# Kernel optimization log

Measured on AMD Instinct MI355X. Metric: run time of the kernel, lower is better.

Reference implementation:

```python
import jax, jax.numpy as jnp
import numpy as np

MUL = 32          # channel multiplicity of node features (32x0e + 32x1o)
N_SPEC = 4        # one-hot species dim (node_attrs = 4x0e)
N_EMB = 8         # radial (bessel) embedding dim
HID = 8           # invariant_neurons
TP_W = 4 * MUL    # tp.weight_numel: 4 'uvu' paths, 32 weights each
INV_SQRT3 = 0.5773502691896258


def setup_inputs() -> dict:
    key = jax.random.key(0)
    ks = jax.random.split(key, 13)
    N, E = 50000, 800000
    node_features = jax.random.normal(ks[0], (N, 4 * MUL), jnp.float32)
    node_attrs = jax.random.uniform(ks[1], (N, N_SPEC), dtype=jnp.float32)
    edge_index = jax.random.randint(ks[2], (2, E), 0, N)
    edge_attrs = jax.random.normal(ks[3], (E, 4), jnp.float32)          # SH: [0e | 1o(3)]
    edge_embedding = jax.random.uniform(ks[4], (E, N_EMB), dtype=jnp.float32)
    # learned parameters
    W1_s = jax.random.normal(ks[5], (MUL, MUL), jnp.float32)            # linear_1 scalar block
    W1_v = jax.random.normal(ks[6], (MUL, MUL), jnp.float32)            # linear_1 vector block
    fc_w1 = jax.random.normal(ks[7], (N_EMB, HID), jnp.float32)         # radial MLP layer 1
    fc_w2 = jax.random.normal(ks[8], (HID, TP_W), jnp.float32)          # radial MLP -> tp weights
    W2_s = jax.random.normal(ks[9], (2 * MUL, MUL), jnp.float32)        # linear_2: 64x0e -> 32x0e
    W2_v = jax.random.normal(ks[10], (2 * MUL, MUL), jnp.float32)       # linear_2: 64x1o -> 32x1o
    Wsc_s = jax.random.normal(ks[11], (MUL, N_SPEC, MUL), jnp.float32)  # sc: 0e x 0e -> 0e (uvw)
    Wsc_v = jax.random.normal(ks[12], (MUL, N_SPEC, MUL), jnp.float32)  # sc: 1o x 0e -> 1o (uvw)
    return dict(node_features=node_features, node_attrs=node_attrs,
                edge_attrs=edge_attrs, edge_embedding=edge_embedding,
                W1_s=W1_s, W1_v=W1_v, fc_w1=fc_w1, fc_w2=fc_w2,
                W2_s=W2_s, W2_v=W2_v, Wsc_s=Wsc_s, Wsc_v=Wsc_v,
                edge_index=edge_index)


def reference(node_features, node_attrs, edge_attrs, edge_embedding,
              W1_s, W1_v, fc_w1, fc_w2, W2_s, W2_v, Wsc_s, Wsc_v, edge_index):
    N = node_features.shape[0]
    edge_src = edge_index[1]
    edge_dst = edge_index[0]

    # split node features into scalar (32x0e) and vector (32x1o) blocks
    s = node_features[:, :MUL]                       # [N, 32]
    v = node_features[:, MUL:].reshape(N, MUL, 3)    # [N, 32, 3]

    # --- self-connection: FullyConnectedTensorProduct(features, node_attrs) ---
    sc_norm = 1.0 / jnp.sqrt(jnp.float32(MUL * N_SPEC))
    sc_s = jnp.einsum('nu,na,uaw->nw', s, node_attrs, Wsc_s) * sc_norm
    sc_v = jnp.einsum('nui,na,uaw->nwi', v, node_attrs, Wsc_v) * sc_norm

    # --- linear_1 (per-irrep linear, fan-in normalized) ---
    l1 = 1.0 / jnp.sqrt(jnp.float32(MUL))
    s1 = (s @ W1_s) * l1                                   # [N, 32]
    v1 = jnp.einsum('nui,uw->nwi', v, W1_v) * l1           # [N, 32, 3]

    # --- radial MLP: edge_embedding -> per-edge tp weights (silu) ---
    h = jax.nn.silu((edge_embedding @ fc_w1) / jnp.sqrt(jnp.float32(N_EMB)))
    w = (h @ fc_w2) / jnp.sqrt(jnp.float32(HID))           # [E, 128]
    w0, w1, w2, w3 = w[:, :MUL], w[:, MUL:2*MUL], w[:, 2*MUL:3*MUL], w[:, 3*MUL:]

    # --- gather source-node features per edge ---
    ss = s1[edge_src]                                      # [E, 32]
    vv = v1[edge_src]                                      # [E, 32, 3]
    a0 = edge_attrs[:, 0]                                  # [E]    0e SH
    a1 = edge_attrs[:, 1:4]                                # [E, 3] 1o SH

    # --- 'uvu' CG tensor product (4 paths) with per-edge weights ---
    o_s0 = w0 * ss * a0[:, None]                                    # 0e x 0e -> 0e
    o_s1 = w3 * jnp.einsum('eui,ei->eu', vv, a1) * INV_SQRT3        # 1o x 1o -> 0e
    o_v0 = w1[:, :, None] * ss[:, :, None] * a1[:, None, :]        # 0e x 1o -> 1o
    o_v1 = w2[:, :, None] * vv * a0[:, None, None]                 # 1o x 0e -> 1o

    eS = jnp.concatenate([o_s0, o_s1], axis=1)             # [E, 64] (64x0e)
    eV = jnp.concatenate([o_v0, o_v1], axis=1)             # [E, 64, 3] (64x1o)

    # --- scatter-add to destination nodes ---
    S = jax.ops.segment_sum(eS, edge_dst, num_segments=N)  # [N, 64]
    V = jax.ops.segment_sum(eV, edge_dst, num_segments=N)  # [N, 64, 3]

    # --- linear_2 (64x0e+64x1o -> 32x0e+32x1o) ---
    l2 = 1.0 / jnp.sqrt(jnp.float32(2 * MUL))
    s_out = (S @ W2_s) * l2
    v_out = jnp.einsum('nui,uw->nwi', V, W2_v) * l2

    # --- residual self-connection ---
    s_out = s_out + sc_s
    v_out = v_out + sc_v
    return jnp.concatenate([s_out, v_out.reshape(N, MUL * 3)], axis=1)  # [N, 128]
```

## Files before the change

### kernel.cpp

```cpp
#include <hip/hip_runtime.h>
#include <math.h>


__device__ __forceinline__ unsigned short f2bf(float x) {
    unsigned u = __float_as_uint(x);
    u += 0x7FFFu + ((u >> 16) & 1u);
    return (unsigned short)(u >> 16);
}
__device__ __forceinline__ float bf2f(unsigned short h) {
    return __uint_as_float(((unsigned)h) << 16);
}

__global__ __launch_bounds__(256) void node_prep(
    const float* __restrict__ nf, const float* __restrict__ W1_s,
    const float* __restrict__ W1_v, const int* __restrict__ eidx,
    int* __restrict__ cnt, ushort* __restrict__ sv1, int N, int E)
{
    __shared__ float w1s[1024];
    __shared__ float w1v[1024];
    __shared__ float nrow[8][128];

    for (long long e = (long long)blockIdx.x * 256 + threadIdx.x; e < E;
         e += (long long)gridDim.x * 256)
        atomicAdd(cnt + eidx[(int)e], 1);

    int g = threadIdx.x >> 5;
    int w = threadIdx.x & 31;
    int n = blockIdx.x * 8 + g;

    for (int i = threadIdx.x; i < 1024; i += 256) {
        w1s[i] = W1_s[i];
        w1v[i] = W1_v[i];
    }
    if (n < N) {
        float4 q = *(const float4*)(nf + (size_t)n * 128 + w * 4);
        *(float4*)&nrow[g][w * 4] = q;
    }
    __syncthreads();
    if (n >= N) return;

    const float l1 = 0.17677669529663687f;
    const float* r = nrow[g];
    float ss = 0.f, vx = 0.f, vy = 0.f, vz = 0.f;
#pragma unroll 8
    for (int u = 0; u < 32; ++u) {
        float ws = w1s[u * 32 + w];
        float wv = w1v[u * 32 + w];
        ss += r[u] * ws;
        vx += r[32 + u * 3 + 0] * wv;
        vy += r[32 + u * 3 + 1] * wv;
        vz += r[32 + u * 3 + 2] * wv;
    }
    ushort4 o;
    o.x = f2bf(ss * l1); o.y = f2bf(vx * l1);
    o.z = f2bf(vy * l1); o.w = f2bf(vz * l1);
    *(ushort4*)(sv1 + (size_t)n * 128 + w * 4) = o;
}


__global__ __launch_bounds__(1024) void scan_a(
    const int* __restrict__ cnt, int* __restrict__ rs,
    int* __restrict__ bsum, int N)
{
    int i = blockIdx.x * 1024 + threadIdx.x;
    int lane = threadIdx.x & 63;
    int wid = threadIdx.x >> 6;
    int v = (i < N) ? cnt[i] : 0;
    int incl = v;
#pragma unroll
    for (int d = 1; d < 64; d <<= 1) {
        int t = __shfl_up(incl, d);
        if (lane >= d) incl += t;
    }
    __shared__ int wtot[16];
    __shared__ int woff[16];
    if (lane == 63) wtot[wid] = incl;
    __syncthreads();
    if (wid == 0) {
        int t = (lane < 16) ? wtot[lane] : 0;
        int s = t;
#pragma unroll
        for (int d = 1; d < 16; d <<= 1) {
            int q = __shfl_up(s, d);
            if (lane >= d) s += q;
        }
        if (lane < 16) woff[lane] = s - t;
        if (lane == 15) bsum[blockIdx.x] = s;
    }
    __syncthreads();
    if (i < N) rs[i] = woff[wid] + incl - v;
}

__global__ __launch_bounds__(64) void scan_b(
    const int* __restrict__ bsum, int* __restrict__ boff, int nb)
{
    int lane = threadIdx.x;
    int carry = 0;
    for (int base = 0; base < nb; base += 64) {
        int i = base + lane;
        int v = (i < nb) ? bsum[i] : 0;
        int s = v;
#pragma unroll
        for (int d = 1; d < 64; d <<= 1) {
            int t = __shfl_up(s, d);
            if (lane >= d) s += t;
        }
        if (i < nb) boff[i] = carry + s - v;
        carry += __shfl(s, 63);
    }
}

__global__ __launch_bounds__(1024) void scan_c(
    int* __restrict__ rs, const int* __restrict__ boff, int N)
{
    int i = blockIdx.x * 1024 + threadIdx.x;
    if (i < N) rs[i] += boff[blockIdx.x];
}

__global__ __launch_bounds__(256) void scatter_kernel(
    const int* __restrict__ eidx, int* __restrict__ rs,
    int* __restrict__ perm, int E)
{
    int e = blockIdx.x * 256 + threadIdx.x;
    if (e < E) {
        int d = eidx[e];
        int p = atomicAdd(rs + d, 1);
        perm[p] = e;
    }
}


__global__ __launch_bounds__(256) void reduce_kernel(
    const float* __restrict__ ea, const float* __restrict__ ee,
    const float* __restrict__ fc1, const float* __restrict__ fc2,
    const ushort* __restrict__ sv1, const int* __restrict__ eidx,
    const int* __restrict__ perm, const int* __restrict__ rs_end,
    const int* __restrict__ cnt, float* __restrict__ SV, int N, int E)
{
    __shared__ float rec[4][64][20];

    int wid = threadIdx.x >> 6;
    int l   = threadIdx.x & 63;
    int h   = l >> 5;
    int u   = l & 31;
    int n = blockIdx.x * 4 + wid;
    if (n >= N) return;

    const float rs8 = 0.35355339059327373f;
    const float inv_sqrt3 = 0.5773502691896258f;

    float f2r[8][4];
#pragma unroll
    for (int k = 0; k < 8; ++k)
#pragma unroll
        for (int j = 0; j < 4; ++j)
            f2r[k][j] = fc2[k * 128 + j * 32 + u];

    int count = cnt[n];
    int start = rs_end[n] - count;

    float aS0 = 0.f, aS1 = 0.f;
    float aV0x = 0.f, aV0y = 0.f, aV0z = 0.f;
    float aV1x = 0.f, aV1y = 0.f, aV1z = 0.f;

    for (int j0 = 0; j0 < count; j0 += 64) {
        int nk = count - j0; if (nk > 64) nk = 64;
        if (l < nk) {
            int e = perm[start + j0 + l];
            const float* eep = ee + (size_t)e * 8;
            float4 e0 = *(const float4*)eep;
            float4 e1 = *(const float4*)(eep + 4);
            float ev[8] = {e0.x, e0.y, e0.z, e0.w, e1.x, e1.y, e1.z, e1.w};
            float hh[8];
#pragma unroll
            for (int k = 0; k < 8; ++k) {
                float t = 0.f;
#pragma unroll
                for (int i = 0; i < 8; ++i) t += ev[i] * fc1[i * 8 + k];
                t *= rs8;
                hh[k] = t * __builtin_amdgcn_rcpf(1.f + __expf(-t)) * rs8;
            }
            float* rr = &rec[wid][l][0];
            *(float4*)rr       = make_float4(hh[0], hh[1], hh[2], hh[3]);
            *(float4*)(rr + 4) = make_float4(hh[4], hh[5], hh[6], hh[7]);
            *(float4*)(rr + 8) = *(const float4*)(ea + (size_t)e * 4);
            rr[12] = __int_as_float(eidx[E + e]);
        }
        int pairs = (nk + 1) >> 1;
        for (int jj = 0; jj < pairs; ++jj) {
            int slot = jj * 2 + h;
            float msk = (slot < nk) ? 1.f : 0.f;
            int slotc = slot < nk ? slot : nk - 1;
            const float* rr = &rec[wid][slotc][0];
            float4 H0 = *(const float4*)rr;
            float4 H1 = *(const float4*)(rr + 4);
            float4 A  = *(const float4*)(rr + 8);
            int src = __float_as_int(rr[12]);
            ushort4 q = *(const ushort4*)(sv1 + (size_t)src * 128 + u * 4);
            float ss = bf2f(q.x) * msk;
            float vx = bf2f(q.y), vy = bf2f(q.z), vz = bf2f(q.w);

            float w0 = H0.x*f2r[0][0] + H0.y*f2r[1][0] + H0.z*f2r[2][0] + H0.w*f2r[3][0]
                     + H1.x*f2r[4][0] + H1.y*f2r[5][0] + H1.z*f2r[6][0] + H1.w*f2r[7][0];
            float w1 = H0.x*f2r[0][1] + H0.y*f2r[1][1] + H0.z*f2r[2][1] + H0.w*f2r[3][1]
                     + H1.x*f2r[4][1] + H1.y*f2r[5][1] + H1.z*f2r[6][1] + H1.w*f2r[7][1];
            float w2 = H0.x*f2r[0][2] + H0.y*f2r[1][2] + H0.z*f2r[2][2] + H0.w*f2r[3][2]
                     + H1.x*f2r[4][2] + H1.y*f2r[5][2] + H1.z*f2r[6][2] + H1.w*f2r[7][2];
            float w3 = H0.x*f2r[0][3] + H0.y*f2r[1][3] + H0.z*f2r[2][3] + H0.w*f2r[3][3]
                     + H1.x*f2r[4][3] + H1.y*f2r[5][3] + H1.z*f2r[6][3] + H1.w*f2r[7][3];

            float dv = (vx * A.y + vy * A.z + vz * A.w) * msk;
            float ssb0 = ss * A.x;
            aS0 += w0 * ssb0;
            aS1 += w3 * dv;
            float c1 = w1 * ss;
            aV0x += c1 * A.y; aV0y += c1 * A.z; aV0z += c1 * A.w;
            float c2 = w2 * A.x * msk;
            aV1x += c2 * vx; aV1y += c2 * vy; aV1z += c2 * vz;
        }
    }

    aS0  += __shfl_xor(aS0, 32);
    aS1  += __shfl_xor(aS1, 32);
    aV0x += __shfl_xor(aV0x, 32);
    aV0y += __shfl_xor(aV0y, 32);
    aV0z += __shfl_xor(aV0z, 32);
    aV1x += __shfl_xor(aV1x, 32);
    aV1y += __shfl_xor(aV1y, 32);
    aV1z += __shfl_xor(aV1z, 32);

    if (h == 0) {
        float* o = SV + (size_t)n * 256 + u * 8;
        *(float4*)o       = make_float4(aS0, aS1 * inv_sqrt3, aV0x, aV0y);
        *(float4*)(o + 4) = make_float4(aV0z, aV1x, aV1y, aV1z);
    }
}


__global__ __launch_bounds__(256) void edge_kernel(
    const float* __restrict__ ea, const float* __restrict__ ee,
    const float* __restrict__ fc1, const float* __restrict__ fc2,
    const ushort* __restrict__ sv1, const int* __restrict__ eidx,
    float* __restrict__ SV, int E)
{
    long long tid = (long long)blockIdx.x * 256 + threadIdx.x;
    int e = (int)(tid >> 5);
    int u = (int)(tid & 31);
    if (e >= E) return;
    const float rs8 = 0.35355339059327373f;
    const float inv_sqrt3 = 0.5773502691896258f;
    float ev[8];
#pragma unroll
    for (int i = 0; i < 8; ++i) ev[i] = ee[(size_t)e * 8 + i];
    float h[8];
#pragma unroll
    for (int k = 0; k < 8; ++k) {
        float t = 0.f;
#pragma unroll
        for (int i = 0; i < 8; ++i) t += ev[i] * fc1[i * 8 + k];
        t *= rs8;
        h[k] = t / (1.f + expf(-t));
    }
    float w0 = 0.f, w1 = 0.f, w2 = 0.f, w3 = 0.f;
#pragma unroll
    for (int k = 0; k < 8; ++k) {
        const float* f2 = fc2 + k * 128;
        float hk = h[k];
        w0 += hk * f2[u];
        w1 += hk * f2[32 + u];
        w2 += hk * f2[64 + u];
        w3 += hk * f2[96 + u];
    }
    w0 *= rs8; w1 *= rs8; w2 *= rs8; w3 *= rs8;
    int dst = eidx[e];
    int src = eidx[E + e];
    float a0 = ea[(size_t)e * 4 + 0];
    float ax = ea[(size_t)e * 4 + 1];
    float ay = ea[(size_t)e * 4 + 2];
    float az = ea[(size_t)e * 4 + 3];
    ushort4 q = *(const ushort4*)(sv1 + (size_t)src * 128 + u * 4);
    float ss = bf2f(q.x), vx = bf2f(q.y), vy = bf2f(q.z), vz = bf2f(q.w);
    float dv = vx * ax + vy * ay + vz * az;
    float* o = SV + (size_t)dst * 256 + u * 8;
    atomicAdd(o + 0, w0 * ss * a0);
    atomicAdd(o + 1, w3 * dv * inv_sqrt3);
    float c1 = w1 * ss;
    atomicAdd(o + 2, c1 * ax);
    atomicAdd(o + 3, c1 * ay);
    atomicAdd(o + 4, c1 * az);
    float c2 = w2 * a0;
    atomicAdd(o + 5, c2 * vx);
    atomicAdd(o + 6, c2 * vy);
    atomicAdd(o + 7, c2 * vz);
}


__global__ __launch_bounds__(256) void node_final(
    const float* __restrict__ SV, const float* __restrict__ W2_s,
    const float* __restrict__ W2_v, const float* __restrict__ nf,
    const float* __restrict__ nattr, const float* __restrict__ Wsc_s,
    const float* __restrict__ Wsc_v, float* __restrict__ out, int N)
{
    __shared__ float wq[4096];
    __shared__ float wsp[4096];
    __shared__ float wvp[4096];
    __shared__ float svt[8][8][32];
    __shared__ float nrow[8][128];

    int g = threadIdx.x >> 5;
    int w = threadIdx.x & 31;

    for (int i = threadIdx.x; i < 1024; i += 256) {
        int uu = i >> 5, ww = i & 31;
        *(float4*)&wq[i * 4] = make_float4(W2_s[i], W2_s[i + 1024],
                                           W2_v[i], W2_v[i + 1024]);
        const float* ps = Wsc_s + (size_t)uu * 128 + ww;
        const float* pv = Wsc_v + (size_t)uu * 128 + ww;
        *(float4*)&wsp[i * 4] = make_float4(ps[0], ps[32], ps[64], ps[96]);
        *(float4*)&wvp[i * 4] = make_float4(pv[0], pv[32], pv[64], pv[96]);
    }
    __syncthreads();

    const float l2 = 0.125f;
    const float sc_norm = 0.08838834764831843f;

    for (int t = 0; t < 4; ++t) {
        int n = blockIdx.x * 32 + g * 4 + t;
        if (n >= N) continue;
        const float* svp = SV + (size_t)n * 256 + w * 8;
        float4 p0 = *(const float4*)svp;
        float4 p1 = *(const float4*)(svp + 4);
        svt[g][0][w] = p0.x; svt[g][1][w] = p0.y;
        svt[g][2][w] = p0.z; svt[g][3][w] = p0.w;
        svt[g][4][w] = p1.x; svt[g][5][w] = p1.y;
        svt[g][6][w] = p1.z; svt[g][7][w] = p1.w;
        float4 q = *(const float4*)(nf + (size_t)n * 128 + w * 4);
        *(float4*)&nrow[g][w * 4] = q;
        float at0 = nattr[(size_t)n * 4 + 0];
        float at1 = nattr[(size_t)n * 4 + 1];
        float at2 = nattr[(size_t)n * 4 + 2];
        float at3 = nattr[(size_t)n * 4 + 3];

        float sa = 0.f, va0 = 0.f, va1 = 0.f, va2 = 0.f;
        float scs = 0.f, scv0 = 0.f, scv1 = 0.f, scv2 = 0.f;
#pragma unroll
        for (int u = 0; u < 32; ++u) {
            float4 qw = *(const float4*)&wq[(u * 32 + w) * 4];
            sa  += svt[g][0][u] * qw.x + svt[g][1][u] * qw.y;
            va0 += svt[g][2][u] * qw.z + svt[g][5][u] * qw.w;
            va1 += svt[g][3][u] * qw.z + svt[g][6][u] * qw.w;
            va2 += svt[g][4][u] * qw.z + svt[g][7][u] * qw.w;
            float4 ps = *(const float4*)&wsp[(u * 32 + w) * 4];
            float4 pv = *(const float4*)&wvp[(u * 32 + w) * 4];
            float cs = at0 * ps.x + at1 * ps.y + at2 * ps.z + at3 * ps.w;
            float cv = at0 * pv.x + at1 * pv.y + at2 * pv.z + at3 * pv.w;
            scs  += nrow[g][u] * cs;
            scv0 += nrow[g][32 + u * 3 + 0] * cv;
            scv1 += nrow[g][32 + u * 3 + 1] * cv;
            scv2 += nrow[g][32 + u * 3 + 2] * cv;
        }
        float* orow = out + (size_t)n * 128;
        orow[w] = sa * l2 + scs * sc_norm;
        orow[32 + w * 3 + 0] = va0 * l2 + scv0 * sc_norm;
        orow[32 + w * 3 + 1] = va1 * l2 + scv1 * sc_norm;
        orow[32 + w * 3 + 2] = va2 * l2 + scv2 * sc_norm;
    }
}

extern "C" void kernel_launch(void* const* d_in, const int* in_sizes, int n_in,
                              void* d_out, int out_size, void* d_ws, size_t ws_size,
                              hipStream_t stream) {
    const float* nf    = (const float*)d_in[0];
    const float* nattr = (const float*)d_in[1];
    const float* ea    = (const float*)d_in[2];
    const float* ee    = (const float*)d_in[3];
    const float* W1_s  = (const float*)d_in[4];
    const float* W1_v  = (const float*)d_in[5];
    const float* fc1   = (const float*)d_in[6];
    const float* fc2   = (const float*)d_in[7];
    const float* W2_s  = (const float*)d_in[8];
    const float* W2_v  = (const float*)d_in[9];
    const float* Wsc_s = (const float*)d_in[10];
    const float* Wsc_v = (const float*)d_in[11];
    const int*   eidx  = (const int*)d_in[12];

    int N = in_sizes[0] / 128;
    int E = in_sizes[12] / 2;

    float* ws = (float*)d_ws;
    ushort* sv1 = (ushort*)ws;
    float* SV  = ws + (size_t)N * 64;
    int* cnt  = (int*)(SV + (size_t)N * 256);
    int* rs   = cnt + N;
    int* bsum = rs + N;
    int* boff = bsum + 64;
    int* perm = boff + 64;

    size_t needed = ((size_t)N * 320 + 2 * (size_t)N + 128 + (size_t)E) * 4;

    int nb_node = (N + 7) / 8;
    int nbE = (E + 255) / 256;
    int nb_final = (N + 31) / 32;

    if (ws_size >= needed) {
        hipMemsetAsync(cnt, 0, (size_t)N * sizeof(int), stream);
        node_prep<<<nb_node, 256, 0, stream>>>(nf, W1_s, W1_v, eidx, cnt, sv1, N, E);
        int nbS = (N + 1023) / 1024;
        scan_a<<<nbS, 1024, 0, stream>>>(cnt, rs, bsum, N);
        scan_b<<<1, 64, 0, stream>>>(bsum, boff, nbS);
        scan_c<<<nbS, 1024, 0, stream>>>(rs, boff, N);
        scatter_kernel<<<nbE, 256, 0, stream>>>(eidx, rs, perm, E);
        int nb_red = (N + 3) / 4;
        reduce_kernel<<<nb_red, 256, 0, stream>>>(ea, ee, fc1, fc2, sv1, eidx,
                                                  perm, rs, cnt, SV, N, E);
        node_final<<<nb_final, 256, 0, stream>>>(SV, W2_s, W2_v, nf, nattr,
                                                 Wsc_s, Wsc_v, (float*)d_out, N);
    } else {
        hipMemsetAsync(SV, 0, (size_t)N * 256 * sizeof(float), stream);
        node_prep<<<nb_node, 256, 0, stream>>>(nf, W1_s, W1_v, eidx, cnt, sv1, N, E);
        long long tot = (long long)E * 32;
        int nb_edge = (int)((tot + 255) / 256);
        edge_kernel<<<nb_edge, 256, 0, stream>>>(ea, ee, fc1, fc2, sv1, eidx, SV, E);
        node_final<<<nb_final, 256, 0, stream>>>(SV, W2_s, W2_v, nf, nattr,
                                                 Wsc_s, Wsc_v, (float*)d_out, N);
    }
}
```

Measured before the change: 262.6 us.

## Fold scan block offsets into consumers, add nontemporal loads, pack radial weights

Removes the scan_c kernel launch by adding the per-1024-block offset inside scatter_kernel and reduce_kernel. Streaming reads and writes of edge index, embedding, attributes, perm and SV are switched to nontemporal loads and stores so they cache less. The radial-weight matvec is regrouped into two-wide float vectors, which may allow packed FMA. These changes save one launch and some cache pollution, at the cost of an extra boff lookup per edge in the scatter.

```diff
diff --git a/kernel.cpp b/kernel.cpp
--- a/kernel.cpp
+++ b/kernel.cpp
@@ -1,6 +1,9 @@
 #include <hip/hip_runtime.h>
 #include <math.h>
 
+
+typedef float  v2f __attribute__((ext_vector_type(2)));
+typedef float  v4f __attribute__((ext_vector_type(4)));
 
 __device__ __forceinline__ unsigned short f2bf(float x) {
     unsigned u = __float_as_uint(x);
@@ -22,7 +25,7 @@
 
     for (long long e = (long long)blockIdx.x * 256 + threadIdx.x; e < E;
          e += (long long)gridDim.x * 256)
-        atomicAdd(cnt + eidx[(int)e], 1);
+        atomicAdd(cnt + __builtin_nontemporal_load(eidx + (int)e), 1);
 
     int g = threadIdx.x >> 5;
     int w = threadIdx.x & 31;
@@ -110,22 +113,15 @@
     }
 }
 
-__global__ __launch_bounds__(1024) void scan_c(
-    int* __restrict__ rs, const int* __restrict__ boff, int N)
-{
-    int i = blockIdx.x * 1024 + threadIdx.x;
-    if (i < N) rs[i] += boff[blockIdx.x];
-}
-
 __global__ __launch_bounds__(256) void scatter_kernel(
     const int* __restrict__ eidx, int* __restrict__ rs,
-    int* __restrict__ perm, int E)
+    const int* __restrict__ boff, int* __restrict__ perm, int E)
 {
     int e = blockIdx.x * 256 + threadIdx.x;
     if (e < E) {
-        int d = eidx[e];
-        int p = atomicAdd(rs + d, 1);
-        perm[p] = e;
+        int d = __builtin_nontemporal_load(eidx + e);
+        int p = atomicAdd(rs + d, 1) + boff[d >> 10];
+        __builtin_nontemporal_store(e, perm + p);
     }
 }
 
@@ -135,7 +131,8 @@
     const float* __restrict__ fc1, const float* __restrict__ fc2,
     const ushort* __restrict__ sv1, const int* __restrict__ eidx,
     const int* __restrict__ perm, const int* __restrict__ rs_end,
-    const int* __restrict__ cnt, float* __restrict__ SV, int N, int E)
+    const int* __restrict__ boff, const int* __restrict__ cnt,
+    float* __restrict__ SV, int N, int E)
 {
     __shared__ float rec[4][64][20];
 
@@ -149,15 +146,17 @@
     const float rs8 = 0.35355339059327373f;
     const float inv_sqrt3 = 0.5773502691896258f;
 
-    float f2r[8][4];
-#pragma unroll
-    for (int k = 0; k < 8; ++k)
-#pragma unroll
-        for (int j = 0; j < 4; ++j)
-            f2r[k][j] = fc2[k * 128 + j * 32 + u];
+    v2f f01[8], f23[8];
+#pragma unroll
+    for (int k = 0; k < 8; ++k) {
+        f01[k].x = fc2[k * 128 + u];
+        f01[k].y = fc2[k * 128 + 32 + u];
+        f23[k].x = fc2[k * 128 + 64 + u];
+        f23[k].y = fc2[k * 128 + 96 + u];
+    }
 
     int count = cnt[n];
-    int start = rs_end[n] - count;
+    int start = rs_end[n] + boff[n >> 10] - count;
 
     float aS0 = 0.f, aS1 = 0.f;
     float aV0x = 0.f, aV0y = 0.f, aV0z = 0.f;
@@ -166,10 +165,9 @@
     for (int j0 = 0; j0 < count; j0 += 64) {
         int nk = count - j0; if (nk > 64) nk = 64;
         if (l < nk) {
-            int e = perm[start + j0 + l];
-            const float* eep = ee + (size_t)e * 8;
-            float4 e0 = *(const float4*)eep;
-            float4 e1 = *(const float4*)(eep + 4);
+            int e = __builtin_nontemporal_load(perm + start + j0 + l);
+            v4f e0 = __builtin_nontemporal_load((const v4f*)(ee + (size_t)e * 8));
+            v4f e1 = __builtin_nontemporal_load((const v4f*)(ee + (size_t)e * 8 + 4));
             float ev[8] = {e0.x, e0.y, e0.z, e0.w, e1.x, e1.y, e1.z, e1.w};
             float hh[8];
 #pragma unroll
@@ -181,10 +179,10 @@
                 hh[k] = t * __builtin_amdgcn_rcpf(1.f + __expf(-t)) * rs8;
             }
             float* rr = &rec[wid][l][0];
-            *(float4*)rr       = make_float4(hh[0], hh[1], hh[2], hh[3]);
-            *(float4*)(rr + 4) = make_float4(hh[4], hh[5], hh[6], hh[7]);
-            *(float4*)(rr + 8) = *(const float4*)(ea + (size_t)e * 4);
-            rr[12] = __int_as_float(eidx[E + e]);
+            *(v4f*)rr       = (v4f){hh[0], hh[1], hh[2], hh[3]};
+            *(v4f*)(rr + 4) = (v4f){hh[4], hh[5], hh[6], hh[7]};
+            *(v4f*)(rr + 8) = __builtin_nontemporal_load((const v4f*)(ea + (size_t)e * 4));
+            rr[12] = __int_as_float(__builtin_nontemporal_load(eidx + E + e));
         }
         int pairs = (nk + 1) >> 1;
         for (int jj = 0; jj < pairs; ++jj) {
@@ -192,30 +190,25 @@
             float msk = (slot < nk) ? 1.f : 0.f;
             int slotc = slot < nk ? slot : nk - 1;
             const float* rr = &rec[wid][slotc][0];
-            float4 H0 = *(const float4*)rr;
-            float4 H1 = *(const float4*)(rr + 4);
-            float4 A  = *(const float4*)(rr + 8);
+            v4f H0 = *(const v4f*)rr;
+            v4f H1 = *(const v4f*)(rr + 4);
+            v4f A  = *(const v4f*)(rr + 8);
             int src = __float_as_int(rr[12]);
             ushort4 q = *(const ushort4*)(sv1 + (size_t)src * 128 + u * 4);
             float ss = bf2f(q.x) * msk;
             float vx = bf2f(q.y), vy = bf2f(q.z), vz = bf2f(q.w);
 
-            float w0 = H0.x*f2r[0][0] + H0.y*f2r[1][0] + H0.z*f2r[2][0] + H0.w*f2r[3][0]
-                     + H1.x*f2r[4][0] + H1.y*f2r[5][0] + H1.z*f2r[6][0] + H1.w*f2r[7][0];
-            float w1 = H0.x*f2r[0][1] + H0.y*f2r[1][1] + H0.z*f2r[2][1] + H0.w*f2r[3][1]
-                     + H1.x*f2r[4][1] + H1.y*f2r[5][1] + H1.z*f2r[6][1] + H1.w*f2r[7][1];
-            float w2 = H0.x*f2r[0][2] + H0.y*f2r[1][2] + H0.z*f2r[2][2] + H0.w*f2r[3][2]
-                     + H1.x*f2r[4][2] + H1.y*f2r[5][2] + H1.z*f2r[6][2] + H1.w*f2r[7][2];
-            float w3 = H0.x*f2r[0][3] + H0.y*f2r[1][3] + H0.z*f2r[2][3] + H0.w*f2r[3][3]
-                     + H1.x*f2r[4][3] + H1.y*f2r[5][3] + H1.z*f2r[6][3] + H1.w*f2r[7][3];
+            v2f w01 = H0.x * f01[0] + H0.y * f01[1] + H0.z * f01[2] + H0.w * f01[3]
+                    + H1.x * f01[4] + H1.y * f01[5] + H1.z * f01[6] + H1.w * f01[7];
+            v2f w23 = H0.x * f23[0] + H0.y * f23[1] + H0.z * f23[2] + H0.w * f23[3]
+                    + H1.x * f23[4] + H1.y * f23[5] + H1.z * f23[6] + H1.w * f23[7];
 
             float dv = (vx * A.y + vy * A.z + vz * A.w) * msk;
-            float ssb0 = ss * A.x;
-            aS0 += w0 * ssb0;
-            aS1 += w3 * dv;
-            float c1 = w1 * ss;
+            aS0 += w01.x * (ss * A.x);
+            aS1 += w23.y * dv;
+            float c1 = w01.y * ss;
             aV0x += c1 * A.y; aV0y += c1 * A.z; aV0z += c1 * A.w;
-            float c2 = w2 * A.x * msk;
+            float c2 = w23.x * A.x * msk;
             aV1x += c2 * vx; aV1y += c2 * vy; aV1z += c2 * vz;
         }
     }
@@ -231,8 +224,8 @@
 
     if (h == 0) {
         float* o = SV + (size_t)n * 256 + u * 8;
-        *(float4*)o       = make_float4(aS0, aS1 * inv_sqrt3, aV0x, aV0y);
-        *(float4*)(o + 4) = make_float4(aV0z, aV1x, aV1y, aV1z);
+        __builtin_nontemporal_store((v4f){aS0, aS1 * inv_sqrt3, aV0x, aV0y}, (v4f*)o);
+        __builtin_nontemporal_store((v4f){aV0z, aV1x, aV1y, aV1z}, (v4f*)(o + 4));
     }
 }
 
@@ -408,11 +401,10 @@
         int nbS = (N + 1023) / 1024;
         scan_a<<<nbS, 1024, 0, stream>>>(cnt, rs, bsum, N);
         scan_b<<<1, 64, 0, stream>>>(bsum, boff, nbS);
-        scan_c<<<nbS, 1024, 0, stream>>>(rs, boff, N);
-        scatter_kernel<<<nbE, 256, 0, stream>>>(eidx, rs, perm, E);
+        scatter_kernel<<<nbE, 256, 0, stream>>>(eidx, rs, boff, perm, E);
         int nb_red = (N + 3) / 4;
         reduce_kernel<<<nb_red, 256, 0, stream>>>(ea, ee, fc1, fc2, sv1, eidx,
-                                                  perm, rs, cnt, SV, N, E);
+                                                  perm, rs, boff, cnt, SV, N, E);
         node_final<<<nb_final, 256, 0, stream>>>(SV, W2_s, W2_v, nf, nattr,
                                                  Wsc_s, Wsc_v, (float*)d_out, N);
     } else {
```

Measured after the change: 294.7 us. +12.2%, slower.
